# Performance work log

Measured on AMD Instinct MI355X. Metric: run time of the kernel, lower is better.

Reference implementation:

```python
import jax, jax.numpy as jnp
import numpy as np

LN_EPS = 1e-5

def _layernorm(x, gamma, beta):
    mu = jnp.mean(x, axis=-1, keepdims=True)
    var = jnp.mean((x - mu) ** 2, axis=-1, keepdims=True)
    return (x - mu) * jax.lax.rsqrt(var + LN_EPS) * gamma + beta

def setup_inputs() -> dict:
    key = jax.random.key(0)
    ks = jax.random.split(key, 12)
    n_drug, n_dis, E = 10000, 10000, 1000000
    feat = 128          # in_units * 2
    d_in = 2 * feat     # in_units * 4 = 256
    hid = 128
    hid2 = hid // 2
    def lin(kw, kb, fan_in, fan_out):
        bound = 1.0 / np.sqrt(fan_in)
        W = jax.random.uniform(kw, (fan_in, fan_out), jnp.float32, -bound, bound)
        b = jax.random.uniform(kb, (fan_out,), jnp.float32, -bound, bound)
        return W, b
    W1, b1 = lin(ks[0], ks[1], d_in, hid)
    W2, b2 = lin(ks[2], ks[3], hid, hid2)
    W3, b3 = lin(ks[4], ks[5], hid2, 1)
    return {
        "drug_feat": jax.random.normal(ks[6], (n_drug, feat), jnp.float32),
        "dis_feat": jax.random.normal(ks[7], (n_dis, feat), jnp.float32),
        "src_idx": jax.random.randint(ks[8], (E,), 0, n_drug, jnp.int32),
        "dst_idx": jax.random.randint(ks[9], (E,), 0, n_dis, jnp.int32),
        "W1": W1, "b1": b1,
        "g1": jnp.ones((hid,), jnp.float32), "be1": jnp.zeros((hid,), jnp.float32),
        "W2": W2, "b2": b2,
        "g2": jnp.ones((hid2,), jnp.float32), "be2": jnp.zeros((hid2,), jnp.float32),
        "W3": W3, "b3": b3,
    }

def reference(drug_feat, dis_feat, src_idx, dst_idx,
              W1, b1, g1, be1, W2, b2, g2, be2, W3, b3):
    # apply_edges: gather src (drug) and dst (disease) features, concat -> [E, 4*in_units]
    m = jnp.concatenate([drug_feat[src_idx], dis_feat[dst_idx]], axis=1)
    h = jax.nn.gelu(_layernorm(m @ W1 + b1, g1, be1), approximate=False)
    h = jax.nn.gelu(_layernorm(h @ W2 + b2, g2, be2), approximate=False)
    return h @ W3 + b3  # [E, 1]
```

## Files before the change

### kernel.cpp

```cpp
#include <hip/hip_runtime.h>
#include <hip/hip_bf16.h>

typedef __attribute__((ext_vector_type(4))) float f32x4;
typedef __attribute__((ext_vector_type(8))) short bf16x8;

#define MFMA16(a, b, c) __builtin_amdgcn_mfma_f32_16x16x32_bf16((a), (b), (c), 0, 0, 0)

#define W1T_OFF 0
#define B1_OFF  65536
#define G1_OFF  66048
#define E1_OFF  66560
#define B2_OFF  67072
#define G2_OFF  67328
#define E2_OFF  67584
#define W3_OFF  67840
#define B3_OFF  68096
#define SMEM_BYTES 68128

__device__ __forceinline__ short f2bf(float x) {
  __hip_bfloat16 h = __float2bfloat16(x);
  return __builtin_bit_cast(short, h);
}

__device__ __forceinline__ bf16x8 pack8(f32x4 a, f32x4 b) {
  bf16x8 r;
  r[0] = f2bf(a[0]); r[1] = f2bf(a[1]); r[2] = f2bf(a[2]); r[3] = f2bf(a[3]);
  r[4] = f2bf(b[0]); r[5] = f2bf(b[1]); r[6] = f2bf(b[2]); r[7] = f2bf(b[3]);
  return r;
}

__device__ __forceinline__ float gelu_fast(float z) {
  float s = z * z;
  float y = z * __builtin_fmaf(-0.10180479f, s, -2.3048496f);
  float t = __builtin_amdgcn_exp2f(y);
  return z * __builtin_amdgcn_rcpf(1.0f + t);
}

__global__ __launch_bounds__(256) void prep_weights(
    const float* __restrict__ W1, const float* __restrict__ W2,
    short* __restrict__ w1i, short* __restrict__ w2L) {
  int idx = blockIdx.x * 256 + threadIdx.x;
  if (idx < 32768) {
    int k = idx >> 7, n = idx & 127;
    w1i[n * 256 + ((((k >> 3) ^ (n & 7)) << 3) | (k & 7))] = f2bf(W1[idx]);
  } else if (idx < 40960) {
    int j = idx - 32768;
    int n = j >> 6, n2 = j & 63;
    int kb2 = n >> 5;
    int qf = (n >> 2) & 3;
    int e = ((n >> 4) & 1) * 4 + (n & 3);
    int t = n2 >> 4, cc2 = n2 & 15;
    w2L[(kb2 * 4 + t) * 512 + (qf * 16 + cc2) * 8 + e] = f2bf(W2[j]);
  }
}

__global__ __launch_bounds__(256) void prep_feats(
    const float* __restrict__ f, short* __restrict__ o, int n8) {
  int idx = blockIdx.x * 256 + threadIdx.x;
  if (idx < n8) {
    f32x4 a = *(const f32x4*)(f + idx * 8);
    f32x4 b = *(const f32x4*)(f + idx * 8 + 4);
    *(bf16x8*)(o + idx * 8) = pack8(a, b);
  }
}

__global__ __launch_bounds__(512, 2) void mlp_fused(
    const short* __restrict__ drugb, const short* __restrict__ disb,
    const int* __restrict__ src, const int* __restrict__ dst,
    const short* __restrict__ w1i, const short* __restrict__ w2L,
    const float* __restrict__ b1, const float* __restrict__ g1, const float* __restrict__ be1,
    const float* __restrict__ b2, const float* __restrict__ g2, const float* __restrict__ be2,
    const float* __restrict__ W3, const float* __restrict__ b3,
    float* __restrict__ out, int E, int ntiles) {
  extern __shared__ char smem[];
  short* w1t = (short*)(smem + W1T_OFF);
  float* b1s = (float*)(smem + B1_OFF);
  float* g1s = (float*)(smem + G1_OFF);
  float* e1s = (float*)(smem + E1_OFF);
  float* b2s = (float*)(smem + B2_OFF);
  float* g2s = (float*)(smem + G2_OFF);
  float* e2s = (float*)(smem + E2_OFF);
  float* w3s = (float*)(smem + W3_OFF);
  float* b3s = (float*)(smem + B3_OFF);

  const int tid  = threadIdx.x;
  const int wave = tid >> 6;
  const int lane = tid & 63;
  const int q    = lane >> 4;
  const int cc   = lane & 15;

  #pragma unroll
  for (int o = 0; o < 8; ++o) {
    int s = (tid + o * 512) * 8;
    *(bf16x8*)(w1t + s) = *(const bf16x8*)(w1i + s);
  }
  if (tid < 128) { b1s[tid] = b1[tid]; g1s[tid] = g1[tid]; e1s[tid] = be1[tid]; }
  else if (tid < 192) { int j = tid - 128; b2s[j] = b2[j]; g2s[j] = g2[j]; e2s[j] = be2[j]; w3s[j] = W3[j]; }
  if (tid == 256) b3s[0] = b3[0];
  __syncthreads();

  const short* w2p = w2L + (lane << 3);

  for (int tile = blockIdx.x; tile < ntiles; tile += gridDim.x) {
    const int r0  = tile * 256 + wave * 32 + cc;
    const int rc0 = (r0 < E) ? r0 : (E - 1);
    const int rc1 = (r0 + 16 < E) ? (r0 + 16) : (E - 1);
    const short* pd0 = drugb + (size_t)src[rc0] * 128 + q * 8;
    const short* pq0 = disb  + (size_t)dst[rc0] * 128 + q * 8;
    const short* pd1 = drugb + (size_t)src[rc1] * 128 + q * 8;
    const short* pq1 = disb  + (size_t)dst[rc1] * 128 + q * 8;

    f32x4 acc1[8][2];
    #pragma unroll
    for (int nt = 0; nt < 8; ++nt) {
      f32x4 bv = *(const f32x4*)(b1s + nt * 16 + q * 4);
      acc1[nt][0] = bv;
      acc1[nt][1] = bv;
    }

    bf16x8 u0 = *(const bf16x8*)pd0;
    bf16x8 u1 = *(const bf16x8*)pd1;
    #pragma unroll 1
    for (int kb = 0; kb < 8; ++kb) {
      bf16x8 f0 = u0, f1 = u1;
      if (kb < 7) {
        const short* pn0 = (kb < 3) ? (pd0 + (kb + 1) * 32) : (pq0 + (kb - 3) * 32);
        const short* pn1 = (kb < 3) ? (pd1 + (kb + 1) * 32) : (pq1 + (kb - 3) * 32);
        u0 = *(const bf16x8*)pn0;
        u1 = *(const bf16x8*)pn1;
      }
      const char* abase = (const char*)w1t + cc * 512 + ((((kb * 4 + q) ^ (cc & 7))) << 4);
      #pragma unroll
      for (int nt = 0; nt < 8; ++nt) {
        bf16x8 af = *(const bf16x8*)(abase + nt * 8192);
        acc1[nt][0] = MFMA16(af, f0, acc1[nt][0]);
        acc1[nt][1] = MFMA16(af, f1, acc1[nt][1]);
      }
    }

    bf16x8 hreg[4][2];
    {
      float s0 = 0.f, ss0 = 0.f, s1 = 0.f, ss1 = 0.f;
      #pragma unroll
      for (int nt = 0; nt < 8; ++nt)
        #pragma unroll
        for (int j = 0; j < 4; ++j) {
          float v0 = acc1[nt][0][j]; s0 += v0; ss0 += v0 * v0;
          float v1 = acc1[nt][1][j]; s1 += v1; ss1 += v1 * v1;
        }
      s0  += __shfl_xor(s0, 16);  s0  += __shfl_xor(s0, 32);
      ss0 += __shfl_xor(ss0, 16); ss0 += __shfl_xor(ss0, 32);
      s1  += __shfl_xor(s1, 16);  s1  += __shfl_xor(s1, 32);
      ss1 += __shfl_xor(ss1, 16); ss1 += __shfl_xor(ss1, 32);
      float mu0 = s0 * 0.0078125f, mu1 = s1 * 0.0078125f;
      float va0 = ss0 * 0.0078125f - mu0 * mu0;
      float va1 = ss1 * 0.0078125f - mu1 * mu1;
      va0 = (va0 > 0.f) ? va0 : 0.f;
      va1 = (va1 > 0.f) ? va1 : 0.f;
      float rs0 = __builtin_amdgcn_rsqf(va0 + 1e-5f);
      float rs1 = __builtin_amdgcn_rsqf(va1 + 1e-5f);

      #pragma unroll
      for (int h = 0; h < 4; ++h) {
        f32x4 glo = *(const f32x4*)(g1s + (2 * h) * 16 + q * 4);
        f32x4 elo = *(const f32x4*)(e1s + (2 * h) * 16 + q * 4);
        f32x4 ghi = *(const f32x4*)(g1s + (2 * h + 1) * 16 + q * 4);
        f32x4 ehi = *(const f32x4*)(e1s + (2 * h + 1) * 16 + q * 4);
        f32x4 a0, b0, a1, b1v;
        #pragma unroll
        for (int j = 0; j < 4; ++j) {
          a0[j]  = gelu_fast(__builtin_fmaf((acc1[2 * h][0][j]     - mu0) * rs0, glo[j], elo[j]));
          b0[j]  = gelu_fast(__builtin_fmaf((acc1[2 * h + 1][0][j] - mu0) * rs0, ghi[j], ehi[j]));
          a1[j]  = gelu_fast(__builtin_fmaf((acc1[2 * h][1][j]     - mu1) * rs1, glo[j], elo[j]));
          b1v[j] = gelu_fast(__builtin_fmaf((acc1[2 * h + 1][1][j] - mu1) * rs1, ghi[j], ehi[j]));
        }
        hreg[h][0] = pack8(a0, b0);
        hreg[h][1] = pack8(a1, b1v);
      }
    }

    f32x4 acc2[4][2];
    #pragma unroll
    for (int t = 0; t < 4; ++t) {
      f32x4 bv = *(const f32x4*)(b2s + t * 16 + q * 4);
      acc2[t][0] = bv;
      acc2[t][1] = bv;
    }

    #pragma unroll
    for (int kb2 = 0; kb2 < 4; ++kb2) {
      bf16x8 h0 = hreg[kb2][0];
      bf16x8 h1 = hreg[kb2][1];
      #pragma unroll
      for (int t = 0; t < 4; ++t) {
        bf16x8 af = *(const bf16x8*)(w2p + (kb2 * 4 + t) * 512);
        acc2[t][0] = MFMA16(af, h0, acc2[t][0]);
        acc2[t][1] = MFMA16(af, h1, acc2[t][1]);
      }
      __builtin_amdgcn_sched_barrier(0);
    }

    {
      float s0 = 0.f, ss0 = 0.f, s1 = 0.f, ss1 = 0.f;
      #pragma unroll
      for (int t = 0; t < 4; ++t)
        #pragma unroll
        for (int j = 0; j < 4; ++j) {
          float v0 = acc2[t][0][j]; s0 += v0; ss0 += v0 * v0;
          float v1 = acc2[t][1][j]; s1 += v1; ss1 += v1 * v1;
        }
      s0  += __shfl_xor(s0, 16);  s0  += __shfl_xor(s0, 32);
      ss0 += __shfl_xor(ss0, 16); ss0 += __shfl_xor(ss0, 32);
      s1  += __shfl_xor(s1, 16);  s1  += __shfl_xor(s1, 32);
      ss1 += __shfl_xor(ss1, 16); ss1 += __shfl_xor(ss1, 32);
      float mu0 = s0 * 0.015625f, mu1 = s1 * 0.015625f;
      float va0 = ss0 * 0.015625f - mu0 * mu0;
      float va1 = ss1 * 0.015625f - mu1 * mu1;
      va0 = (va0 > 0.f) ? va0 : 0.f;
      va1 = (va1 > 0.f) ? va1 : 0.f;
      float rs0 = __builtin_amdgcn_rsqf(va0 + 1e-5f);
      float rs1 = __builtin_amdgcn_rsqf(va1 + 1e-5f);

      float dot0 = 0.f, dot1 = 0.f;
      #pragma unroll
      for (int t = 0; t < 4; ++t) {
        f32x4 gv = *(const f32x4*)(g2s + t * 16 + q * 4);
        f32x4 ev = *(const f32x4*)(e2s + t * 16 + q * 4);
        f32x4 wv = *(const f32x4*)(w3s + t * 16 + q * 4);
        #pragma unroll
        for (int j = 0; j < 4; ++j) {
          float z0 = __builtin_fmaf((acc2[t][0][j] - mu0) * rs0, gv[j], ev[j]);
          float z1 = __builtin_fmaf((acc2[t][1][j] - mu1) * rs1, gv[j], ev[j]);
          dot0 = __builtin_fmaf(gelu_fast(z0), wv[j], dot0);
          dot1 = __builtin_fmaf(gelu_fast(z1), wv[j], dot1);
        }
      }
      dot0 += __shfl_xor(dot0, 16); dot0 += __shfl_xor(dot0, 32);
      dot1 += __shfl_xor(dot1, 16); dot1 += __shfl_xor(dot1, 32);
      if (q == 0) {
        float bias3 = b3s[0];
        if (r0 < E)      out[r0]      = dot0 + bias3;
        if (r0 + 16 < E) out[r0 + 16] = dot1 + bias3;
      }
    }
  }
}

extern "C" void kernel_launch(void* const* d_in, const int* in_sizes, int n_in,
                              void* d_out, int out_size, void* d_ws, size_t ws_size,
                              hipStream_t stream) {
  const float* drug = (const float*)d_in[0];
  const float* dis  = (const float*)d_in[1];
  const int*   src  = (const int*)d_in[2];
  const int*   dst  = (const int*)d_in[3];
  const float* W1   = (const float*)d_in[4];
  const float* b1   = (const float*)d_in[5];
  const float* g1   = (const float*)d_in[6];
  const float* be1  = (const float*)d_in[7];
  const float* W2   = (const float*)d_in[8];
  const float* b2   = (const float*)d_in[9];
  const float* g2   = (const float*)d_in[10];
  const float* be2  = (const float*)d_in[11];
  const float* W3   = (const float*)d_in[12];
  const float* b3   = (const float*)d_in[13];
  float* out = (float*)d_out;

  const int E      = in_sizes[2];
  const int ndrug8 = in_sizes[0] / 8;
  const int ndis8  = in_sizes[1] / 8;
  const int ntiles = (E + 255) / 256;

  short* w1i   = (short*)d_ws;
  short* w2L   = w1i + 32768;
  short* drugb = w2L + 8192;
  short* disb  = drugb + (size_t)ndrug8 * 8;

  (void)hipFuncSetAttribute((const void*)mlp_fused,
                            hipFuncAttributeMaxDynamicSharedMemorySize, SMEM_BYTES);

  prep_weights<<<dim3(160), dim3(256), 0, stream>>>(W1, W2, w1i, w2L);
  prep_feats<<<dim3((ndrug8 + 255) / 256), dim3(256), 0, stream>>>(drug, drugb, ndrug8);
  prep_feats<<<dim3((ndis8 + 255) / 256), dim3(256), 0, stream>>>(dis, disb, ndis8);

  int grid = 512;
  if (ntiles < grid) grid = ntiles;
  mlp_fused<<<dim3(grid), dim3(512), SMEM_BYTES, stream>>>(
      drugb, disb, src, dst, w1i, w2L,
      b1, g1, be1, b2, g2, be2, W3, b3, out, E, ntiles);
}
```

Measured before the change: 237.7 us.

## Prefetch next-tile indices and batch feature gathers with deeper lookahead

The next tile's src/dst indices are now loaded during the current tile, and all four drug-feature chunks are issued at the start of each tile. The disease chunks are then loaded during the first four MFMA steps of a fully unrolled K loop. This aims to hide the dependent index-then-feature gather latency behind compute. Occupancy hint drops from 2 to 1 blocks per CU to make room for the extra registers, and the layernorm affine is folded into one FMA per element. The cost is more register pressure and possibly lower occupancy for latency hiding.

```diff
diff --git a/kernel.cpp b/kernel.cpp
--- a/kernel.cpp
+++ b/kernel.cpp
@@ -64,7 +64,7 @@
   }
 }
 
-__global__ __launch_bounds__(512, 2) void mlp_fused(
+__global__ __launch_bounds__(512, 1) void mlp_fused(
     const short* __restrict__ drugb, const short* __restrict__ disb,
     const int* __restrict__ src, const int* __restrict__ dst,
     const short* __restrict__ w1i, const short* __restrict__ w2L,
@@ -101,14 +101,37 @@
 
   const short* w2p = w2L + (lane << 3);
 
+  int s0i = 0, d0i = 0, s1i = 0, d1i = 0;
+  {
+    int r0 = blockIdx.x * 256 + wave * 32 + cc;
+    int rc0 = (r0 < E) ? r0 : (E - 1);
+    int rc1 = (r0 + 16 < E) ? (r0 + 16) : (E - 1);
+    s0i = src[rc0]; d0i = dst[rc0]; s1i = src[rc1]; d1i = dst[rc1];
+  }
+
   for (int tile = blockIdx.x; tile < ntiles; tile += gridDim.x) {
-    const int r0  = tile * 256 + wave * 32 + cc;
-    const int rc0 = (r0 < E) ? r0 : (E - 1);
-    const int rc1 = (r0 + 16 < E) ? (r0 + 16) : (E - 1);
-    const short* pd0 = drugb + (size_t)src[rc0] * 128 + q * 8;
-    const short* pq0 = disb  + (size_t)dst[rc0] * 128 + q * 8;
-    const short* pd1 = drugb + (size_t)src[rc1] * 128 + q * 8;
-    const short* pq1 = disb  + (size_t)dst[rc1] * 128 + q * 8;
+    const int r0 = tile * 256 + wave * 32 + cc;
+    const short* pd0 = drugb + (size_t)s0i * 128 + q * 8;
+    const short* pq0 = disb  + (size_t)d0i * 128 + q * 8;
+    const short* pd1 = drugb + (size_t)s1i * 128 + q * 8;
+    const short* pq1 = disb  + (size_t)d1i * 128 + q * 8;
+
+    bf16x8 u[4][2];
+    #pragma unroll
+    for (int i = 0; i < 4; ++i) {
+      u[i][0] = *(const bf16x8*)(pd0 + i * 32);
+      u[i][1] = *(const bf16x8*)(pd1 + i * 32);
+    }
+
+    {
+      int tn = tile + gridDim.x;
+      if (tn < ntiles) {
+        int rn  = tn * 256 + wave * 32 + cc;
+        int rcn0 = (rn < E) ? rn : (E - 1);
+        int rcn1 = (rn + 16 < E) ? (rn + 16) : (E - 1);
+        s0i = src[rcn0]; d0i = dst[rcn0]; s1i = src[rcn1]; d1i = dst[rcn1];
+      }
+    }
 
     f32x4 acc1[8][2];
     #pragma unroll
@@ -118,16 +141,13 @@
       acc1[nt][1] = bv;
     }
 
-    bf16x8 u0 = *(const bf16x8*)pd0;
-    bf16x8 u1 = *(const bf16x8*)pd1;
-    #pragma unroll 1
+    #pragma unroll
     for (int kb = 0; kb < 8; ++kb) {
-      bf16x8 f0 = u0, f1 = u1;
-      if (kb < 7) {
-        const short* pn0 = (kb < 3) ? (pd0 + (kb + 1) * 32) : (pq0 + (kb - 3) * 32);
-        const short* pn1 = (kb < 3) ? (pd1 + (kb + 1) * 32) : (pq1 + (kb - 3) * 32);
-        u0 = *(const bf16x8*)pn0;
-        u1 = *(const bf16x8*)pn1;
+      bf16x8 f0 = u[kb & 3][0];
+      bf16x8 f1 = u[kb & 3][1];
+      if (kb < 4) {
+        u[kb & 3][0] = *(const bf16x8*)(pq0 + kb * 32);
+        u[kb & 3][1] = *(const bf16x8*)(pq1 + kb * 32);
       }
       const char* abase = (const char*)w1t + cc * 512 + ((((kb * 4 + q) ^ (cc & 7))) << 4);
       #pragma unroll
@@ -166,13 +186,21 @@
         f32x4 elo = *(const f32x4*)(e1s + (2 * h) * 16 + q * 4);
         f32x4 ghi = *(const f32x4*)(g1s + (2 * h + 1) * 16 + q * 4);
         f32x4 ehi = *(const f32x4*)(e1s + (2 * h + 1) * 16 + q * 4);
+        f32x4 al0, cl0, al1, cl1, ah0, ch0, ah1, ch1;
+        #pragma unroll
+        for (int j = 0; j < 4; ++j) {
+          al0[j] = glo[j] * rs0; cl0[j] = __builtin_fmaf(-mu0, al0[j], elo[j]);
+          al1[j] = glo[j] * rs1; cl1[j] = __builtin_fmaf(-mu1, al1[j], elo[j]);
+          ah0[j] = ghi[j] * rs0; ch0[j] = __builtin_fmaf(-mu0, ah0[j], ehi[j]);
+          ah1[j] = ghi[j] * rs1; ch1[j] = __builtin_fmaf(-mu1, ah1[j], ehi[j]);
+        }
         f32x4 a0, b0, a1, b1v;
         #pragma unroll
         for (int j = 0; j < 4; ++j) {
-          a0[j]  = gelu_fast(__builtin_fmaf((acc1[2 * h][0][j]     - mu0) * rs0, glo[j], elo[j]));
-          b0[j]  = gelu_fast(__builtin_fmaf((acc1[2 * h + 1][0][j] - mu0) * rs0, ghi[j], ehi[j]));
-          a1[j]  = gelu_fast(__builtin_fmaf((acc1[2 * h][1][j]     - mu1) * rs1, glo[j], elo[j]));
-          b1v[j] = gelu_fast(__builtin_fmaf((acc1[2 * h + 1][1][j] - mu1) * rs1, ghi[j], ehi[j]));
+          a0[j]  = gelu_fast(__builtin_fmaf(acc1[2 * h][0][j],     al0[j], cl0[j]));
+          b0[j]  = gelu_fast(__builtin_fmaf(acc1[2 * h + 1][0][j], ah0[j], ch0[j]));
+          a1[j]  = gelu_fast(__builtin_fmaf(acc1[2 * h][1][j],     al1[j], cl1[j]));
+          b1v[j] = gelu_fast(__builtin_fmaf(acc1[2 * h + 1][1][j], ah1[j], ch1[j]));
         }
         hreg[h][0] = pack8(a0, b0);
         hreg[h][1] = pack8(a1, b1v);
```

After: 234.6 us. About the same (-1.3%).
